# Optimization experiments

Hardware: AMD Instinct MI355X
Metric: run time of the kernel (lower is better)

Reference implementation:

```python
import jax, jax.numpy as jnp
import numpy as np

D_MODEL = 1024
N_HEADS = 16
SPARSITY_FACTOR = 4  # band half-width
HEAD_DIM = D_MODEL // N_HEADS
SCALE = HEAD_DIM ** (-0.5)


def _band_mask(seq_len: int, stride: int) -> jnp.ndarray:
    # mask[i, j] = True iff max(0, i-stride) <= j <= min(S-1, i+stride)
    i = jnp.arange(seq_len)[:, None]
    j = jnp.arange(seq_len)[None, :]
    return jnp.abs(i - j) <= stride


def setup_inputs() -> dict:
    key = jax.random.key(0)
    kq, kk, kv = jax.random.split(key, 3)
    B, S = 256, 128
    q = jax.random.normal(kq, (B, S, D_MODEL), dtype=jnp.float32)
    k = jax.random.normal(kk, (B, S, D_MODEL), dtype=jnp.float32)
    v = jax.random.normal(kv, (B, S, D_MODEL), dtype=jnp.float32)
    return {"q": q, "k": k, "v": v}


def reference(q, k, v):
    B, S, _ = q.shape
    # [B, S, D] -> [B, H, S, Dh]
    qh = q.reshape(B, S, N_HEADS, HEAD_DIM).transpose(0, 2, 1, 3)
    kh = k.reshape(B, S, N_HEADS, HEAD_DIM).transpose(0, 2, 1, 3)
    vh = v.reshape(B, S, N_HEADS, HEAD_DIM).transpose(0, 2, 1, 3)
    # dense scores, then banded mask (faithful to original)
    scores = jnp.einsum("bhqd,bhkd->bhqk", qh, kh) * SCALE  # [B,H,S,S]
    mask = _band_mask(S, SPARSITY_FACTOR)  # [S,S] bool
    scores = jnp.where(mask, scores, -jnp.inf)
    weights = jax.nn.softmax(scores, axis=-1)
    out = jnp.einsum("bhqk,bhkd->bhqd", weights, vh)  # [B,H,S,Dh]
    return out.transpose(0, 2, 1, 3).reshape(B, S, D_MODEL)
```

## Files before the change

kernel.cpp:

```cpp
#include <hip/hip_runtime.h>

#define SEQ   128
#define DM    1024
#define NH    16
#define HD    64
#define BAND  4
#define WIN   9
#define SCALE 0.125f

__device__ __forceinline__ float wave_sum64(float x) {
#define DPP_ADD(ctrl)                                                          \
  x += __int_as_float(                                                         \
      __builtin_amdgcn_update_dpp(0, __float_as_int(x), ctrl, 0xf, 0xf, true));
  DPP_ADD(0x111)
  DPP_ADD(0x112)
  DPP_ADD(0x114)
  DPP_ADD(0x118)
  DPP_ADD(0x142)
  DPP_ADD(0x143)
#undef DPP_ADD
  return x;
}

__global__ __launch_bounds__(256, 8)
void banded_attn(const float* __restrict__ q, const float* __restrict__ k,
                 const float* __restrict__ v, float* __restrict__ out) {
  const int lane = threadIdx.x & 63;
  const int wid  = (blockIdx.x << 2) | (threadIdx.x >> 6);
  const int half = wid & 1;
  const int bh   = wid >> 1;
  const int h    = bh & (NH - 1);
  const int b    = bh >> 4;

  const size_t base = (size_t)b * (SEQ * DM) + (size_t)h * HD + lane;
  const float* qp = q + base;
  const float* kp = k + base;
  const float* vp = v + base;
  float*       op = out + base;

  const int i0 = half * 64;

  float kw[WIN], vw[WIN];
#pragma unroll
  for (int t = 0; t < WIN; ++t) { kw[t] = 0.f; vw[t] = 0.f; }

#pragma unroll
  for (int t = 0; t < WIN - 1; ++t) {
    int j = i0 - BAND + t;
    if (j >= 0) {
      kw[t] = kp[(size_t)j * DM];
      vw[t] = vp[(size_t)j * DM];
    }
  }

  const float* qrow = qp + (size_t)i0 * DM;
  const float* krow = kp + (size_t)(i0 + BAND) * DM;
  const float* vrow = vp + (size_t)(i0 + BAND) * DM;
  float*       orow = op + (size_t)i0 * DM;

  for (int i = i0; i < i0 + 64; ++i) {
    if (i + BAND < SEQ) {
      kw[WIN - 1] = *krow;
      vw[WIN - 1] = *vrow;
    }
    const float qd = *qrow;

    float sum = 0.f, o = 0.f;
#pragma unroll
    for (int t = 0; t < WIN; ++t) {
      const unsigned j = (unsigned)(i - BAND + t);
      if (j < SEQ) {
        const float r = wave_sum64(qd * kw[t]);
        const float s =
            SCALE * __int_as_float(__builtin_amdgcn_readlane(__float_as_int(r), 63));
        const float e = __expf(s);
        sum += e;
        o += e * vw[t];
      }
    }
    const float inv = 1.0f / sum;
    *orow = o * inv;

#pragma unroll
    for (int t = 0; t < WIN - 1; ++t) { kw[t] = kw[t + 1]; vw[t] = vw[t + 1]; }

    qrow += DM; krow += DM; vrow += DM; orow += DM;
  }
}

extern "C" void kernel_launch(void* const* d_in, const int* in_sizes, int n_in,
                              void* d_out, int out_size, void* d_ws, size_t ws_size,
                              hipStream_t stream) {
  const float* q = (const float*)d_in[0];
  const float* k = (const float*)d_in[1];
  const float* v = (const float*)d_in[2];
  float* out = (float*)d_out;

  dim3 grid(2048), block(256);
  hipLaunchKernelGGL(banded_attn, grid, block, 0, stream, q, k, v, out);
}
```

Measured before the change: 435.9 us.

## Stage K/V per head in swizzled LDS and compute one query row per thread

Replaces the wave-per-half-sequence design, which did a cross-lane DPP reduction for every score, with one block per (batch, head) where each thread owns a query row held in registers. K is staged into a 32KB XOR-swizzled LDS tile with float4 loads, scores are computed as per-thread dot products, then the same tile is reused for V to build the output. This removes the per-score wave reductions and readlanes and vectorises global loads. In exchange it needs heavy register use (64 floats of q per thread), small 128-thread blocks, and strided per-thread row stores of q and out.

```diff
diff --git a/kernel.cpp b/kernel.cpp
--- a/kernel.cpp
+++ b/kernel.cpp
@@ -8,83 +8,91 @@
 #define WIN   9
 #define SCALE 0.125f
 
-__device__ __forceinline__ float wave_sum64(float x) {
-#define DPP_ADD(ctrl)                                                          \
-  x += __int_as_float(                                                         \
-      __builtin_amdgcn_update_dpp(0, __float_as_int(x), ctrl, 0xf, 0xf, true));
-  DPP_ADD(0x111)
-  DPP_ADD(0x112)
-  DPP_ADD(0x114)
-  DPP_ADD(0x118)
-  DPP_ADD(0x142)
-  DPP_ADD(0x143)
-#undef DPP_ADD
-  return x;
+__device__ __forceinline__ int swz(int j, int c) {
+  return (j << 6) + ((c ^ (j & 15)) << 2);
 }
 
-__global__ __launch_bounds__(256, 8)
+__global__ __launch_bounds__(128, 2)
 void banded_attn(const float* __restrict__ q, const float* __restrict__ k,
                  const float* __restrict__ v, float* __restrict__ out) {
-  const int lane = threadIdx.x & 63;
-  const int wid  = (blockIdx.x << 2) | (threadIdx.x >> 6);
-  const int half = wid & 1;
-  const int bh   = wid >> 1;
-  const int h    = bh & (NH - 1);
-  const int b    = bh >> 4;
+  __shared__ __align__(16) float tile[SEQ * HD];
 
-  const size_t base = (size_t)b * (SEQ * DM) + (size_t)h * HD + lane;
-  const float* qp = q + base;
-  const float* kp = k + base;
-  const float* vp = v + base;
-  float*       op = out + base;
+  const int tid = threadIdx.x;
+  const int bh  = blockIdx.x;
+  const int h   = bh & (NH - 1);
+  const int b   = bh >> 4;
 
-  const int i0 = half * 64;
-
-  float kw[WIN], vw[WIN];
-#pragma unroll
-  for (int t = 0; t < WIN; ++t) { kw[t] = 0.f; vw[t] = 0.f; }
+  const size_t hbase = (size_t)b * (SEQ * DM) + (size_t)h * HD;
+  const float4* kg = (const float4*)(k + hbase);
+  const float4* vg = (const float4*)(v + hbase);
+  float4*       tl = (float4*)tile;
 
 #pragma unroll
-  for (int t = 0; t < WIN - 1; ++t) {
-    int j = i0 - BAND + t;
-    if (j >= 0) {
-      kw[t] = kp[(size_t)j * DM];
-      vw[t] = vp[(size_t)j * DM];
-    }
+  for (int m = 0; m < 16; ++m) {
+    const int g = (m << 7) + tid;
+    const int j = g >> 4, c = g & 15;
+    tl[swz(j, c) >> 2] = kg[j * 256 + c];
   }
 
-  const float* qrow = qp + (size_t)i0 * DM;
-  const float* krow = kp + (size_t)(i0 + BAND) * DM;
-  const float* vrow = vp + (size_t)(i0 + BAND) * DM;
-  float*       orow = op + (size_t)i0 * DM;
+  const float4* qg = (const float4*)(q + hbase + (size_t)tid * DM);
+  float4 qr[16];
+#pragma unroll
+  for (int c = 0; c < 16; ++c) qr[c] = qg[c];
 
-  for (int i = i0; i < i0 + 64; ++i) {
-    if (i + BAND < SEQ) {
-      kw[WIN - 1] = *krow;
-      vw[WIN - 1] = *vrow;
+  __syncthreads();
+
+  float e[WIN];
+  float sum = 0.f;
+#pragma unroll
+  for (int t = 0; t < WIN; ++t) {
+    const int  j     = tid - BAND + t;
+    const bool valid = (unsigned)j < SEQ;
+    const int  jc    = valid ? j : 0;
+    float s = 0.f;
+#pragma unroll
+    for (int c = 0; c < 16; ++c) {
+      const float4 k4 = tl[swz(jc, c) >> 2];
+      s += qr[c].x * k4.x + qr[c].y * k4.y + qr[c].z * k4.z + qr[c].w * k4.w;
     }
-    const float qd = *qrow;
+    const float ev = valid ? __expf(s * SCALE) : 0.f;
+    e[t] = ev;
+    sum += ev;
+  }
+  const float inv = 1.0f / sum;
+#pragma unroll
+  for (int t = 0; t < WIN; ++t) e[t] *= inv;
 
-    float sum = 0.f, o = 0.f;
+  __syncthreads();
+
+#pragma unroll
+  for (int m = 0; m < 16; ++m) {
+    const int g = (m << 7) + tid;
+    const int j = g >> 4, c = g & 15;
+    tl[swz(j, c) >> 2] = vg[j * 256 + c];
+  }
+  __syncthreads();
+
+  int rb[WIN], pm[WIN];
+#pragma unroll
+  for (int t = 0; t < WIN; ++t) {
+    const int j  = tid - BAND + t;
+    const int jc = ((unsigned)j < SEQ) ? j : 0;
+    rb[t] = jc << 6;
+    pm[t] = jc & 15;
+  }
+  float4* og = (float4*)(out + hbase + (size_t)tid * DM);
+#pragma unroll
+  for (int c = 0; c < 16; ++c) {
+    float4 o = {0.f, 0.f, 0.f, 0.f};
 #pragma unroll
     for (int t = 0; t < WIN; ++t) {
-      const unsigned j = (unsigned)(i - BAND + t);
-      if (j < SEQ) {
-        const float r = wave_sum64(qd * kw[t]);
-        const float s =
-            SCALE * __int_as_float(__builtin_amdgcn_readlane(__float_as_int(r), 63));
-        const float e = __expf(s);
-        sum += e;
-        o += e * vw[t];
-      }
+      const float4 v4 = tl[(rb[t] + ((c ^ pm[t]) << 2)) >> 2];
+      o.x += e[t] * v4.x;
+      o.y += e[t] * v4.y;
+      o.z += e[t] * v4.z;
+      o.w += e[t] * v4.w;
     }
-    const float inv = 1.0f / sum;
-    *orow = o * inv;
-
-#pragma unroll
-    for (int t = 0; t < WIN - 1; ++t) { kw[t] = kw[t + 1]; vw[t] = vw[t + 1]; }
-
-    qrow += DM; krow += DM; vrow += DM; orow += DM;
+    og[c] = o;
   }
 }
 
@@ -96,6 +104,6 @@
   const float* v = (const float*)d_in[2];
   float* out = (float*)d_out;
 
-  dim3 grid(2048), block(256);
+  dim3 grid(256 * NH), block(128);
   hipLaunchKernelGGL(banded_attn, grid, block, 0, stream, q, k, v, out);
 }
```

After: 471.5 us. 1.08x slower.
